# Performance work log

Measured on AMD Instinct MI355X. Metric: run time of the kernel, lower is better.

## Reference

```python
import jax, jax.numpy as jnp
import numpy as np

B, NEIGH, D = 512, 16, 128
N_ENT, N_REL, K = 100000, 64, 4


def setup_inputs() -> dict:
    key = jax.random.key(0)
    k1, k2, k3, k4, k5, k6, k7 = jax.random.split(key, 7)
    M = B * NEIGH
    return {
        "mol_emb": jax.random.normal(k1, (B, D), dtype=jnp.float32),
        "entity_emb": jax.random.normal(k2, (N_ENT, D), dtype=jnp.float32),
        "relation_emb": jax.random.normal(k3, (N_REL, D), dtype=jnp.float32),
        "relation_matrix": jax.random.normal(k4, (N_REL, D, D), dtype=jnp.float32) / jnp.sqrt(jnp.float32(D)),
        "tail_ids": jax.random.randint(k5, (B, NEIGH), 0, N_ENT),
        "rel_ids": jax.random.randint(k6, (B, NEIGH), 0, N_REL),
        "neg_indices": jax.random.randint(k7, (M, K), 0, M),
    }


def reference(mol_emb, entity_emb, relation_emb, relation_matrix, tail_ids, rel_ids, neg_indices):
    t_ids = tail_ids.reshape(-1)           # [M]
    r_ids = rel_ids.reshape(-1)            # [M]
    M = t_ids.shape[0]
    n = M // mol_emb.shape[0]

    neigh_emb = entity_emb[t_ids]          # [M, D] gather
    rel_e = relation_emb[r_ids]            # [M, D] gather
    rel_m = relation_matrix[r_ids]         # [M, D, D] gather (dominant traffic)

    # tile self embedding per neighbor: [B,1,D] -> [B,n,D] -> [M,D]
    self_e = jnp.repeat(mol_emb, n, axis=0)

    Rh = jnp.einsum('mij,mj->mi', rel_m, self_e)     # batched GEMV
    Rt = jnp.einsum('mij,mj->mi', rel_m, neigh_emb)
    pos_score = jnp.sum(jnp.square(Rh + rel_e - Rt), axis=-1)  # [M]

    # negatives: same head/relation per triple, corrupted tails from neigh_emb
    neg_emb = neigh_emb[neg_indices.reshape(-1)].reshape(M, K, D)
    # Rh_neg == Rh (same relation matrix, same self vector)
    Rt_neg = jnp.einsum('mij,mkj->mki', rel_m, neg_emb)        # [M, K, D]
    neg_score = jnp.sum(jnp.square(Rh[:, None, :] + rel_e[:, None, :] - Rt_neg), axis=-1)  # [M, K]

    pos_loss = pos_score.reshape(-1, n)                         # [B, n]
    neg_loss = jnp.mean(neg_score, axis=-1).reshape(-1, n)      # [B, n]
    loss = -jnp.log(jax.nn.sigmoid(neg_loss - pos_loss) + 1e-12)
    return jnp.mean(jnp.sum(loss, axis=-1))
```

## Files before the change

### kernel.cpp

```cpp
#include <hip/hip_runtime.h>
#include <math.h>

#define BATCH  512
#define NEIGH  16
#define DIM    128
#define NEG_K  4
#define M_TOT  (BATCH * NEIGH)
#define NREL   64
#define SLICES 8
#define TPP    16
#define MAXT   2
#define BCAP   256

typedef __attribute__((ext_vector_type(8))) short short8;
typedef __attribute__((ext_vector_type(4))) float f32x4;

static __device__ __forceinline__ unsigned short f2bf(float x) {
    unsigned u = __float_as_uint(x);
    u += 0x7FFFu + ((u >> 16) & 1u);
    return (unsigned short)(u >> 16);
}


__global__ __launch_bounds__(256) void kg_scatter(const int* __restrict__ tail,
                                                  const int* __restrict__ rel,
                                                  const int* __restrict__ neg,
                                                  int* __restrict__ wsi) {
    const int m = blockIdx.x * 256 + threadIdx.x;
    const int r = rel[m];
    const int pos = atomicAdd(&wsi[r], 1);
    if (pos >= BCAP) return;
    const int4 nv = *(const int4*)(neg + 4 * m);
    const int4 a = { m, tail[m], tail[nv.x], tail[nv.y] };
    const int4 b = { tail[nv.z], tail[nv.w], 0, 0 };
    int* slot = wsi + 64 + ((((r << 8) + pos)) << 3);
    *(int4*)slot       = a;
    *((int4*)slot + 1) = b;
}

__global__ __launch_bounds__(256)
void kg_main(const float* __restrict__ mol,
             const float* __restrict__ ent,
             const float* __restrict__ rele,
             const float* __restrict__ relm,
             const int*   __restrict__ wsi,
             float*       __restrict__ out) {
    const int tid = threadIdx.x;
    const int r   = blockIdx.x >> 3;
    const int s   = blockIdx.x & 7;

    int cnt = wsi[r];
    if (cnt > BCAP) cnt = BCAP;
    const int ntiles = (cnt + TPP - 1) / TPP;
    if (s >= ntiles) return;
    int L = 1 + (ntiles - 1 - s) / SLICES;
    if (L > MAXT) L = MAXT;

    __shared__ __align__(16) unsigned short Al[DIM * DIM];
    __shared__ __align__(16) unsigned short Bl[5 * TPP * DIM];
    __shared__ float reL[DIM];
    __shared__ int   idb[MAXT][TPP][8];
    __shared__ float wpart[4][TPP][5];
    __shared__ float lloss;

    if (tid == 0) lloss = 0.0f;

    const int* bucket = wsi + 64 + ((r << 8) << 3);
    for (int idx = tid; idx < L * TPP * 8; idx += 256) {
        const int l   = idx >> 7;
        const int rem = idx & 127;
        const int tt  = rem >> 3;
        const int fld = rem & 7;
        int p = (s + l * SLICES) * TPP + tt;
        if (p >= cnt) p = 0;
        idb[l][tt][fld] = bucket[p * 8 + fld];
    }

    const float* Rg = relm + (size_t)r * DIM * DIM;
    #pragma unroll
    for (int it = 0; it < 16; ++it) {
        const int f   = tid + (it << 8);
        const int row = f >> 5;
        const int c4  = f & 31;
        const float4 q = *(const float4*)(Rg + row * DIM + c4 * 4);
        uint2 u;
        u.x = (unsigned)f2bf(q.x) | ((unsigned)f2bf(q.y) << 16);
        u.y = (unsigned)f2bf(q.z) | ((unsigned)f2bf(q.w) << 16);
        const int byteoff = (row << 8) + ((c4 << 3) ^ ((row & 7) << 4));
        *(uint2*)((char*)Al + byteoff) = u;
    }
    if (tid < DIM) reL[tid] = rele[r * DIM + tid];
    __syncthreads();

    auto stageB = [&](int l) {
        #pragma unroll
        for (int it = 0; it < 20; ++it) {
            const int f   = tid + (it << 8);
            const int row = f >> 6;
            const int v   = row >> 4;
            const int tt  = row & 15;
            const int k2  = f & 63;
            const int m0  = idb[l][tt][0];
            const int hid = m0 >> 4;
            const int eid = idb[l][tt][1 + v];
            const float2 h2 = *(const float2*)(mol + ((size_t)hid << 7) + (k2 << 1));
            const float2 t2 = *(const float2*)(ent + ((size_t)eid << 7) + (k2 << 1));
            const unsigned pk = (unsigned)f2bf(h2.x - t2.x) |
                                ((unsigned)f2bf(h2.y - t2.y) << 16);
            const int byteoff = (row << 8) + ((k2 << 2) ^ ((row & 7) << 4));
            *(unsigned*)((char*)Bl + byteoff) = pk;
        }
    };
    stageB(0);

    const int lane = tid & 63;
    const int w    = tid >> 6;
    const int g    = lane >> 4;
    const int c    = lane & 15;
    const int swz  = (lane & 7) << 4;
    const f32x4 zz = {0.f, 0.f, 0.f, 0.f};

    for (int l = 0; l < L; ++l) {
        __syncthreads();

        float rre[2][4];
        #pragma unroll
        for (int mt = 0; mt < 2; ++mt)
            #pragma unroll
            for (int q = 0; q < 4; ++q)
                rre[mt][q] = reL[((w * 2 + mt) << 4) + (g << 2) + q];

        f32x4 acc[2][5];
        #pragma unroll
        for (int mt = 0; mt < 2; ++mt)
            #pragma unroll
            for (int v = 0; v < 5; ++v) acc[mt][v] = zz;

        #pragma unroll
        for (int kk = 0; kk < 4; ++kk) {
            short8 af[2];
            #pragma unroll
            for (int mt = 0; mt < 2; ++mt) {
                const int row = ((w * 2 + mt) << 4) + c;
                af[mt] = *(const short8*)((const char*)Al + (row << 8) +
                                          (((kk << 6) + (g << 4)) ^ swz));
            }
            #pragma unroll
            for (int v = 0; v < 5; ++v) {
                const int rb = (v << 4) + c;
                const short8 bf = *(const short8*)((const char*)Bl + (rb << 8) +
                                                   (((kk << 6) + (g << 4)) ^ swz));
                acc[0][v] = __builtin_amdgcn_mfma_f32_16x16x32_bf16(af[0], bf, acc[0][v], 0, 0, 0);
                acc[1][v] = __builtin_amdgcn_mfma_f32_16x16x32_bf16(af[1], bf, acc[1][v], 0, 0, 0);
            }
        }

        float part[5];
        #pragma unroll
        for (int v = 0; v < 5; ++v) {
            float p2 = 0.f;
            #pragma unroll
            for (int mt = 0; mt < 2; ++mt)
                #pragma unroll
                for (int q = 0; q < 4; ++q) {
                    const float z = acc[mt][v][q] + rre[mt][q];
                    p2 = fmaf(z, z, p2);
                }
            p2 += __shfl_xor(p2, 16, 64);
            p2 += __shfl_xor(p2, 32, 64);
            part[v] = p2;
        }
        if (lane < 16) {
            #pragma unroll
            for (int v = 0; v < 5; ++v) wpart[w][lane][v] = part[v];
        }
        __syncthreads();

        const int tb = (s + l * SLICES) * TPP;
        if (tid < 16 && tid < cnt - tb) {
            float pos = 0.f, n1 = 0.f, n2 = 0.f, n3 = 0.f, n4 = 0.f;
            #pragma unroll
            for (int w2 = 0; w2 < 4; ++w2) {
                pos += wpart[w2][tid][0];
                n1  += wpart[w2][tid][1];
                n2  += wpart[w2][tid][2];
                n3  += wpart[w2][tid][3];
                n4  += wpart[w2][tid][4];
            }
            const float x  = 0.25f * (n1 + n2 + n3 + n4) - pos;
            const float sg = 1.0f / (1.0f + expf(-x));
            const float lv = -logf(sg + 1e-12f);
            atomicAdd(&lloss, lv);
        }

        if (l + 1 < L) stageB(l + 1);
    }

    __syncthreads();
    if (tid == 0) atomicAdd(out, lloss * (1.0f / (float)BATCH));
}

extern "C" void kernel_launch(void* const* d_in, const int* in_sizes, int n_in,
                              void* d_out, int out_size, void* d_ws, size_t ws_size,
                              hipStream_t stream) {
    const float* mol  = (const float*)d_in[0];
    const float* ent  = (const float*)d_in[1];
    const float* rele = (const float*)d_in[2];
    const float* relm = (const float*)d_in[3];
    const int*   tail = (const int*)d_in[4];
    const int*   rel  = (const int*)d_in[5];
    const int*   neg  = (const int*)d_in[6];
    float* out = (float*)d_out;
    int*   wsi = (int*)d_ws;

    hipMemsetAsync(wsi, 0, NREL * sizeof(int), stream);
    hipMemsetAsync(out, 0, sizeof(float), stream);
    kg_scatter<<<M_TOT / 256, 256, 0, stream>>>(tail, rel, neg, wsi);
    kg_main<<<NREL * SLICES, 256, 0, stream>>>(mol, ent, rele, relm, wsi, out);
}
```

Before: 126.5 us.

## Fuse relation bucketing into main kernel via per-block rel scan and prefix sum

Drops the separate scatter kernel and its workspace memset. Each block of the main kernel now scans all 8192 relation ids, builds a prefix sum in shared memory and picks out the triples for its own relation and slice. This removes two launches, the global atomics and the workspace round trip. In exchange, every one of the 512 blocks re-reads the whole rel array and runs a 256-wide scan with 16 barriers before its real work starts. The ordering within each bucket also becomes deterministic.

```diff
diff --git a/kernel.cpp b/kernel.cpp
--- a/kernel.cpp
+++ b/kernel.cpp
@@ -10,7 +10,6 @@
 #define SLICES 8
 #define TPP    16
 #define MAXT   2
-#define BCAP   256
 
 typedef __attribute__((ext_vector_type(8))) short short8;
 typedef __attribute__((ext_vector_type(4))) float f32x4;
@@ -21,59 +20,80 @@
     return (unsigned short)(u >> 16);
 }
 
-
-__global__ __launch_bounds__(256) void kg_scatter(const int* __restrict__ tail,
-                                                  const int* __restrict__ rel,
-                                                  const int* __restrict__ neg,
-                                                  int* __restrict__ wsi) {
-    const int m = blockIdx.x * 256 + threadIdx.x;
-    const int r = rel[m];
-    const int pos = atomicAdd(&wsi[r], 1);
-    if (pos >= BCAP) return;
-    const int4 nv = *(const int4*)(neg + 4 * m);
-    const int4 a = { m, tail[m], tail[nv.x], tail[nv.y] };
-    const int4 b = { tail[nv.z], tail[nv.w], 0, 0 };
-    int* slot = wsi + 64 + ((((r << 8) + pos)) << 3);
-    *(int4*)slot       = a;
-    *((int4*)slot + 1) = b;
-}
-
 __global__ __launch_bounds__(256)
-void kg_main(const float* __restrict__ mol,
-             const float* __restrict__ ent,
-             const float* __restrict__ rele,
-             const float* __restrict__ relm,
-             const int*   __restrict__ wsi,
-             float*       __restrict__ out) {
+void kg_fused(const float* __restrict__ mol,
+              const float* __restrict__ ent,
+              const float* __restrict__ rele,
+              const float* __restrict__ relm,
+              const int*   __restrict__ tail,
+              const int*   __restrict__ rel,
+              const int*   __restrict__ neg,
+              float*       __restrict__ out) {
     const int tid = threadIdx.x;
     const int r   = blockIdx.x >> 3;
     const int s   = blockIdx.x & 7;
 
-    int cnt = wsi[r];
-    if (cnt > BCAP) cnt = BCAP;
+    __shared__ __align__(16) unsigned short Al[DIM * DIM];
+    __shared__ __align__(16) unsigned short Bl[5 * TPP * DIM];
+    __shared__ float reL[DIM];
+    __shared__ int   idb[MAXT][TPP][8];
+    __shared__ int   pfx[256];
+    __shared__ float wpart[4][TPP][5];
+    __shared__ float lloss;
+
+    ((int*)idb)[tid] = 0;
+    if (tid == 0) lloss = 0.0f;
+
+    const int  base = tid << 5;
+    const int4* rp  = (const int4*)(rel + base);
+    unsigned mask = 0;
+    int cnt_t = 0;
+    #pragma unroll
+    for (int i = 0; i < 8; ++i) {
+        const int4 v = rp[i];
+        if (v.x == r) { mask |= 1u << (4 * i + 0); ++cnt_t; }
+        if (v.y == r) { mask |= 1u << (4 * i + 1); ++cnt_t; }
+        if (v.z == r) { mask |= 1u << (4 * i + 2); ++cnt_t; }
+        if (v.w == r) { mask |= 1u << (4 * i + 3); ++cnt_t; }
+    }
+    pfx[tid] = cnt_t;
+    __syncthreads();
+    #pragma unroll
+    for (int off = 1; off < 256; off <<= 1) {
+        const int v = (tid >= off) ? pfx[tid - off] : 0;
+        __syncthreads();
+        pfx[tid] += v;
+        __syncthreads();
+    }
+    int cnt = pfx[255];
+    if (cnt > 256) cnt = 256;
     const int ntiles = (cnt + TPP - 1) / TPP;
     if (s >= ntiles) return;
     int L = 1 + (ntiles - 1 - s) / SLICES;
     if (L > MAXT) L = MAXT;
 
-    __shared__ __align__(16) unsigned short Al[DIM * DIM];
-    __shared__ __align__(16) unsigned short Bl[5 * TPP * DIM];
-    __shared__ float reL[DIM];
-    __shared__ int   idb[MAXT][TPP][8];
-    __shared__ float wpart[4][TPP][5];
-    __shared__ float lloss;
-
-    if (tid == 0) lloss = 0.0f;
-
-    const int* bucket = wsi + 64 + ((r << 8) << 3);
-    for (int idx = tid; idx < L * TPP * 8; idx += 256) {
-        const int l   = idx >> 7;
-        const int rem = idx & 127;
-        const int tt  = rem >> 3;
-        const int fld = rem & 7;
-        int p = (s + l * SLICES) * TPP + tt;
-        if (p >= cnt) p = 0;
-        idb[l][tt][fld] = bucket[p * 8 + fld];
+    {
+        int rk = pfx[tid] - cnt_t;
+        unsigned mm = mask;
+        while (mm) {
+            const int i = __builtin_ctz(mm); mm &= mm - 1;
+            const int t = rk >> 4;
+            if ((t & 7) == s) {
+                const int l = t >> 3;
+                if (l < L) {
+                    const int tt = rk & 15;
+                    const int m  = base + i;
+                    const int4 nv = *(const int4*)(neg + 4 * m);
+                    idb[l][tt][0] = m;
+                    idb[l][tt][1] = tail[m];
+                    idb[l][tt][2] = tail[nv.x];
+                    idb[l][tt][3] = tail[nv.y];
+                    idb[l][tt][4] = tail[nv.z];
+                    idb[l][tt][5] = tail[nv.w];
+                }
+            }
+            ++rk;
+        }
     }
 
     const float* Rg = relm + (size_t)r * DIM * DIM;
@@ -211,10 +231,7 @@
     const int*   rel  = (const int*)d_in[5];
     const int*   neg  = (const int*)d_in[6];
     float* out = (float*)d_out;
-    int*   wsi = (int*)d_ws;
-
-    hipMemsetAsync(wsi, 0, NREL * sizeof(int), stream);
+
     hipMemsetAsync(out, 0, sizeof(float), stream);
-    kg_scatter<<<M_TOT / 256, 256, 0, stream>>>(tail, rel, neg, wsi);
-    kg_main<<<NREL * SLICES, 256, 0, stream>>>(mol, ent, rele, relm, wsi, out);
+    kg_fused<<<NREL * SLICES, 256, 0, stream>>>(mol, ent, rele, relm, tail, rel, neg, out);
 }
```

New measurement: 114.0 us. 1.11x faster.
